# Kernel tuning notes

Hardware: AMD Instinct MI355X
Metric: run time of the kernel (lower is better)

## Reference

```python
import jax, jax.numpy as jnp
import numpy as np

B, CH, H, W = 32, 128, 32, 32
EMB = 64      # embedding_dim
NEMB = 8192   # codebook size


def setup_inputs() -> dict:
    key = jax.random.key(0)
    k1, k2, k3, k4 = jax.random.split(key, 4)
    z = jax.random.normal(k1, (B, CH, H, W), jnp.float32)
    # 1x1 conv == per-pixel linear: weight [EMB, CH], bias [EMB]
    proj_w = jax.random.normal(k2, (EMB, CH), jnp.float32) * 0.05
    proj_b = jax.random.normal(k3, (EMB,), jnp.float32) * 0.01
    embed_w = jax.random.normal(k4, (NEMB, EMB), jnp.float32)
    return {"z": z, "proj_w": proj_w, "proj_b": proj_b, "embed_w": embed_w}


def reference(z, proj_w, proj_b, embed_w):
    Bz, C, Hh, Ww = z.shape
    sg = jax.lax.stop_gradient
    # 1x1 conv then permute(0,2,3,1): [B,C,H,W] -> [B,H,W,E]
    z_e = jnp.einsum('bchw,ec->bhwe', z, proj_w) + proj_b
    flat = z_e.reshape(-1, z_e.shape[-1])  # [N, E], N = B*H*W
    dist = ((flat * flat).sum(1, keepdims=True)
            - 2.0 * (flat @ embed_w.T)
            + (embed_w * embed_w).sum(1)[None, :])
    z_q_ind = jnp.argmin(dist, axis=1).reshape(Bz, Hh, Ww)  # argmax(-dist)
    z_q_emb = embed_w[z_q_ind]  # gather: [B,H,W,E]
    commitment_cost = 0.25
    kld_scale = 10.0
    latent_loss = kld_scale * (
        commitment_cost * jnp.mean((sg(z_q_emb) - z_e) ** 2)
        + jnp.mean((z_q_emb - sg(z_e)) ** 2))
    z_q_flat = z_q_emb
    # straight-through estimator
    z_q_st = z_e + sg(z_q_emb - z_e)
    out = jnp.transpose(z_q_st, (0, 3, 1, 2))  # [B,E,H,W]
    return out, z_q_flat, latent_loss, z_q_ind
```

## Files before the change

kernel.cpp:

```cpp
#include <hip/hip_runtime.h>

#define NPIX   32768
#define NEMB_  8192
#define EMB_   64
#define CH_    128
#define CAPP   768

#define OUT_OFF  0
#define ZQ_OFF   2097152
#define LOSS_OFF 4194304
#define IND_OFF  4194305

typedef _Float16 h8   __attribute__((ext_vector_type(8)));
typedef float    f16f __attribute__((ext_vector_type(16)));

__global__ __launch_bounds__(256) void k_wpack(
    const float* __restrict__ ew, const float* __restrict__ pw,
    float4* __restrict__ W4, float* __restrict__ pwT,
    float* __restrict__ wsq, float* __restrict__ wsqp,
    float* __restrict__ lacc, int* __restrict__ done)
{
    const int tid = threadIdx.x;
    {
        const int i = blockIdx.x * 256 + tid;
        const float v = pw[i];
        const int e = i >> 7, c = i & 127;
        pwT[c * 64 + e] = v;
    }
    const int m = blockIdx.x * 256 + tid;
    const float4* wr = (const float4*)(ew + (size_t)m * EMB_);
    float w[EMB_];
    float s = 0.f;
    #pragma unroll
    for (int i = 0; i < 16; i++) {
        float4 v = wr[i];
        w[4*i] = v.x; w[4*i+1] = v.y; w[4*i+2] = v.z; w[4*i+3] = v.w;
        s += v.x*v.x + v.y*v.y + v.z*v.z + v.w*v.w;
    }
    wsq[m] = s;
    float sh = (float)(_Float16)s;
    float sl = s - sh;
    const int t  = m >> 5;
    const int li = m & 31;
    #pragma unroll
    for (int s5 = 0; s5 < 4; s5++) {
        #pragma unroll
        for (int h = 0; h < 2; h++) {
            h8 hh;
            #pragma unroll
            for (int j = 0; j < 8; j++) hh[j] = (_Float16)w[s5 * 16 + h * 8 + j];
            W4[(size_t)(t * 5 + s5) * 64 + h * 32 + li] = __builtin_bit_cast(float4, hh);
        }
    }
    {
        h8 hh;
        #pragma unroll
        for (int j = 0; j < 8; j++) hh[j] = (_Float16)0.f;
        hh[0] = (_Float16)sh; hh[1] = (_Float16)sl;
        W4[(size_t)(t * 5 + 4) * 64 + 0 * 32 + li] = __builtin_bit_cast(float4, hh);
        #pragma unroll
        for (int j = 0; j < 8; j++) hh[j] = (_Float16)0.f;
        W4[(size_t)(t * 5 + 4) * 64 + 1 * 32 + li] = __builtin_bit_cast(float4, hh);
    }
    __shared__ float red[256];
    red[tid] = s;
    __syncthreads();
    for (int o = 128; o > 0; o >>= 1) {
        if (tid < o) red[tid] = fmaxf(red[tid], red[tid + o]);
        __syncthreads();
    }
    if (tid == 0) wsqp[blockIdx.x] = red[0];
    if (blockIdx.x == 0 && tid == 0) { *lacc = 0.f; *done = 0; }
}

__device__ __forceinline__ unsigned long long pack_key(float d, int m)
{
    unsigned fb = __float_as_uint(d);
    fb ^= ((int)fb < 0) ? 0xFFFFFFFFu : 0x80000000u;
    return ((unsigned long long)fb << 32) | (unsigned)m;
}

__global__ __launch_bounds__(1024, 4) void k_fused3(
    const float4* __restrict__ W4, const float* __restrict__ z,
    const float* __restrict__ pwT, const float* __restrict__ pb,
    const float* __restrict__ wsqp, const float* __restrict__ wsq,
    const float* __restrict__ ew,
    float* __restrict__ out, float* __restrict__ lacc, int* __restrict__ done)
{
    __shared__ __align__(16) float xs[128][68];
    __shared__ float s1s[1024], s2s[1024], s3s[1024];
    __shared__ short i1s[1024], i2s[1024];
    __shared__ float xsqp_s[8][128];
    __shared__ float thr_s[128];
    __shared__ int   pairs[CAPP];
    __shared__ unsigned long long pbest[128];
    __shared__ int   winner_s[128];
    __shared__ int   smask[128];
    __shared__ float wred[16];
    __shared__ int   npair_s;
    __shared__ float wm_s;

    const int tid  = threadIdx.x;
    const int wv   = tid >> 6;
    const int lane = tid & 63;
    const int n0   = blockIdx.x * 128;
    const int hlf  = lane >> 5;

    if (tid == 0) npair_s = 0;
    if (tid < 128) { smask[tid] = 0; pbest[tid] = ~0ULL; }
    if (tid < 32) {
        float w = wsqp[tid];
        #pragma unroll
        for (int o = 16; o > 0; o >>= 1) w = fmaxf(w, __shfl_xor(w, o));
        if (tid == 0) wm_s = w;
    }

    {
        const int oct = tid >> 7;
        const int pxp = tid & 127;
        const int e0  = __builtin_amdgcn_readfirstlane(oct << 3);
        const float* zp = z + (size_t)(n0 >> 10) * (CH_ * 1024) + (n0 & 1023) + pxp;
        float acc[8];
        #pragma unroll
        for (int j = 0; j < 8; j++) acc[j] = 0.f;
        #pragma unroll 8
        for (int c = 0; c < CH_; c++) {
            const float zv = zp[(size_t)c * 1024];
            const float4* wr = (const float4*)(pwT + c * 64 + e0);
            float4 w0 = wr[0], w1 = wr[1];
            acc[0] = fmaf(zv, w0.x, acc[0]); acc[1] = fmaf(zv, w0.y, acc[1]);
            acc[2] = fmaf(zv, w0.z, acc[2]); acc[3] = fmaf(zv, w0.w, acc[3]);
            acc[4] = fmaf(zv, w1.x, acc[4]); acc[5] = fmaf(zv, w1.y, acc[5]);
            acc[6] = fmaf(zv, w1.z, acc[6]); acc[7] = fmaf(zv, w1.w, acc[7]);
        }
        const float4* pb4 = (const float4*)(pb + e0);
        float4 b0 = pb4[0], b1 = pb4[1];
        acc[0] += b0.x; acc[1] += b0.y; acc[2] += b0.z; acc[3] += b0.w;
        acc[4] += b1.x; acc[5] += b1.y; acc[6] += b1.z; acc[7] += b1.w;
        float sq = 0.f;
        #pragma unroll
        for (int j = 0; j < 8; j++) sq += acc[j] * acc[j];
        ((float4*)&xs[pxp][0])[oct * 2]     = make_float4(acc[0], acc[1], acc[2], acc[3]);
        ((float4*)&xs[pxp][0])[oct * 2 + 1] = make_float4(acc[4], acc[5], acc[6], acc[7]);
        xsqp_s[oct][pxp] = sq;
    }
    __syncthreads();

    const int ch = wv & 7;
    const int pg = wv >> 3;

    h8 bfr[2][4];
    #pragma unroll
    for (int j = 0; j < 2; j++) {
        const int px = pg * 64 + j * 32 + (lane & 31);
        #pragma unroll
        for (int s5 = 0; s5 < 4; s5++) {
            float4 u0 = *(const float4*)(&xs[px][s5 * 16 + hlf * 8]);
            float4 u1 = *(const float4*)(&xs[px][s5 * 16 + hlf * 8 + 4]);
            h8 hh;
            hh[0]=(_Float16)u0.x; hh[1]=(_Float16)u0.y; hh[2]=(_Float16)u0.z; hh[3]=(_Float16)u0.w;
            hh[4]=(_Float16)u1.x; hh[5]=(_Float16)u1.y; hh[6]=(_Float16)u1.z; hh[7]=(_Float16)u1.w;
            bfr[j][s5] = hh;
        }
    }
    h8 btail;
    {
        h8 hh;
        #pragma unroll
        for (int q = 0; q < 8; q++) hh[q] = (_Float16)0.f;
        if (hlf == 0) { hh[0] = (_Float16)-0.5f; hh[1] = (_Float16)-0.5f; }
        btail = hh;
    }

    const f16f kzero = {0,0,0,0,0,0,0,0,0,0,0,0,0,0,0,0};
    float s1[2], s2[2], s3[2];
    int   i1[2], i2[2];
    #pragma unroll
    for (int j = 0; j < 2; j++) { s1[j]=s2[j]=s3[j]=-3.0e38f; i1[j]=i2[j]=0; }

    const int tb = ch * 32;
    const float4* Wb = W4 + (size_t)tb * 320 + lane;
    float4 A[5];
    #pragma unroll
    for (int s = 0; s < 5; s++) A[s] = Wb[s * 64];

#define REDUCE_J(ACC, JJ, GT)                                                  \
    {                                                                          \
        float t0 = fmaxf(fmaxf(ACC[0],  ACC[1]),  ACC[2]);                     \
        float t1 = fmaxf(fmaxf(ACC[3],  ACC[4]),  ACC[5]);                     \
        float t2 = fmaxf(fmaxf(ACC[6],  ACC[7]),  ACC[8]);                     \
        float t3 = fmaxf(fmaxf(ACC[9],  ACC[10]), ACC[11]);                    \
        float t4 = fmaxf(fmaxf(ACC[12], ACC[13]), ACC[14]);                    \
        float v  = fmaxf(fmaxf(fmaxf(t0, t1), fmaxf(t2, t3)),                  \
                         fmaxf(t4, ACC[15]));                                  \
        v = fmaxf(v, __shfl_xor(v, 32));                                       \
        bool c1 = v > s1[JJ];                                                  \
        bool c2 = v > s2[JJ];                                                  \
        int  cand = c1 ? i1[JJ] : (GT);                                        \
        i2[JJ] = c2 ? cand : i2[JJ];                                           \
        s3[JJ] = fmaxf(fminf(s2[JJ], v), s3[JJ]);                              \
        s3[JJ] = fminf(s3[JJ], fmaxf(s2[JJ], v));                              \
        s2[JJ] = fmaxf(fminf(s1[JJ], v), fminf(s2[JJ], fmaxf(s1[JJ], v)));     \
        i1[JJ] = c1 ? (GT) : i1[JJ];                                           \
        s1[JJ] = fmaxf(s1[JJ], v);                                             \
    }

    for (int tt = 0; tt < 32; tt++) {
        const int gt = tb + tt;
        f16f acc0 = __builtin_amdgcn_mfma_f32_32x32x16_f16(
            __builtin_bit_cast(h8, A[0]), bfr[0][0], kzero, 0, 0, 0);
        #pragma unroll
        for (int s = 1; s < 4; s++)
            acc0 = __builtin_amdgcn_mfma_f32_32x32x16_f16(
                __builtin_bit_cast(h8, A[s]), bfr[0][s], acc0, 0, 0, 0);
        acc0 = __builtin_amdgcn_mfma_f32_32x32x16_f16(
            __builtin_bit_cast(h8, A[4]), btail, acc0, 0, 0, 0);
        REDUCE_J(acc0, 0, gt)
        f16f acc1 = __builtin_amdgcn_mfma_f32_32x32x16_f16(
            __builtin_bit_cast(h8, A[0]), bfr[1][0], kzero, 0, 0, 0);
        #pragma unroll
        for (int s = 1; s < 4; s++)
            acc1 = __builtin_amdgcn_mfma_f32_32x32x16_f16(
                __builtin_bit_cast(h8, A[s]), bfr[1][s], acc1, 0, 0, 0);
        acc1 = __builtin_amdgcn_mfma_f32_32x32x16_f16(
            __builtin_bit_cast(h8, A[4]), btail, acc1, 0, 0, 0);
        {
            const int tp = (tt + 1) < 32 ? (tt + 1) : 31;
            const float4* wp = Wb + (size_t)tp * 320;
            #pragma unroll
            for (int s = 0; s < 5; s++) A[s] = wp[s * 64];
        }
        REDUCE_J(acc1, 1, gt)
    }
#undef REDUCE_J

    if (lane < 32) {
        #pragma unroll
        for (int j = 0; j < 2; j++) {
            const int px = pg * 64 + j * 32 + lane;
            const int cell = px * 8 + ch;
            s1s[cell] = s1[j]; s2s[cell] = s2[j]; s3s[cell] = s3[j];
            i1s[cell] = (short)i1[j]; i2s[cell] = (short)i2[j];
        }
    }
    __syncthreads();

    if (tid < 128) {
        float s1g = s1s[tid * 8];
        #pragma unroll
        for (int c = 1; c < 8; c++) s1g = fmaxf(s1g, s1s[tid * 8 + c]);
        float xq = xsqp_s[0][tid];
        #pragma unroll
        for (int o = 1; o < 8; o++) xq += xsqp_s[o][tid];
        float E = 0.00125f * sqrtf(xq * wm_s) + 1e-5f * wm_s + 3e-4f;
        thr_s[tid] = s1g - 2.0f * E;
    }
    __syncthreads();
    {
        const int cell = tid;
        const int px = cell >> 3, chh = cell & 7;
        const float th = thr_s[px];
        const float cs1 = s1s[cell], cs2 = s2s[cell], cs3 = s3s[cell];
        if (cs3 >= th) {
            int pos = atomicAdd(&npair_s, 32);
            if (pos + 32 <= CAPP) {
                for (int t = 0; t < 32; t++)
                    pairs[pos + t] = (px << 8) | (chh * 32 + t);
            } else {
                for (int t = 0; t < 32; t++)
                    if (pos + t < CAPP) pairs[pos + t] = -1;
                smask[px] = 1;
            }
        } else {
            if (cs1 >= th) {
                int pos = atomicAdd(&npair_s, 1);
                if (pos < CAPP) pairs[pos] = (px << 8) | (int)i1s[cell];
                else smask[px] = 1;
            }
            if (cs2 >= th) {
                int pos = atomicAdd(&npair_s, 1);
                if (pos < CAPP) pairs[pos] = (px << 8) | (int)i2s[cell];
                else smask[px] = 1;
            }
        }
    }
    __syncthreads();
    const int np = npair_s < CAPP ? npair_s : CAPP;

    const int lg = lane >> 4;
    const int ld = lane & 15;
    for (int i = wv; i < np; i += 16) {
        const int pr = pairs[i];
        if (pr < 0) continue;
        const int p = pr >> 8;
        if (smask[p]) continue;
        const int t = pr & 255;
        const float4* tb4 = (const float4*)(ew + (size_t)t * 2048);
        float4 wq[8];
        #pragma unroll
        for (int q = 0; q < 8; q++) wq[q] = tb4[q * 64 + lane];
        const float4 xq = *(const float4*)(&xs[p][ld * 4]);
        unsigned long long best = ~0ULL;
        #pragma unroll
        for (int q = 0; q < 8; q++) {
            float dp = wq[q].x*xq.x + wq[q].y*xq.y + wq[q].z*xq.z + wq[q].w*xq.w;
            dp += __shfl_xor(dp, 1);
            dp += __shfl_xor(dp, 2);
            dp += __shfl_xor(dp, 4);
            dp += __shfl_xor(dp, 8);
            const int m = t * 32 + q * 4 + lg;
            unsigned long long key = pack_key(fmaf(-2.f, dp, wsq[m]), m);
            best = key < best ? key : best;
        }
        { unsigned long long o = __shfl_xor(best, 16); best = o < best ? o : best; }
        { unsigned long long o = __shfl_xor(best, 32); best = o < best ? o : best; }
        if (lane == 0) atomicMin(&pbest[p], best);
    }
    for (int p = wv; p < 128; p += 16) {
        if (!smask[p]) continue;
        const float4 xq = *(const float4*)(&xs[p][ld * 4]);
        unsigned long long bk = ~0ULL;
        for (int t = 0; t < 256; t++) {
            const float4* tb4 = (const float4*)(ew + (size_t)t * 2048);
            #pragma unroll
            for (int q = 0; q < 8; q++) {
                float4 wv4 = tb4[q * 64 + lane];
                float dp = wv4.x*xq.x + wv4.y*xq.y + wv4.z*xq.z + wv4.w*xq.w;
                dp += __shfl_xor(dp, 1);
                dp += __shfl_xor(dp, 2);
                dp += __shfl_xor(dp, 4);
                dp += __shfl_xor(dp, 8);
                const int m = t * 32 + q * 4 + lg;
                unsigned long long key = pack_key(fmaf(-2.f, dp, wsq[m]), m);
                bk = key < bk ? key : bk;
            }
        }
        { unsigned long long o = __shfl_xor(bk, 16); bk = o < bk ? o : bk; }
        { unsigned long long o = __shfl_xor(bk, 32); bk = o < bk ? o : bk; }
        if (lane == 0) atomicMin(&pbest[p], bk);
    }
    __syncthreads();
    if (tid < 128) {
        const int win = (int)(unsigned)(pbest[tid] & 0xFFFFFFFFULL);
        winner_s[tid] = win;
        out[IND_OFF + n0 + tid] = (float)win;
    }
    __syncthreads();
    float lsum = 0.f;
    {
        const int px = tid >> 3, sg = tid & 7;
        const int win = winner_s[px];
        const float4* wr = (const float4*)(ew + (size_t)win * EMB_ + sg * 8);
        float4* xr  = (float4*)(&xs[px][sg * 8]);
        float4* zq4 = (float4*)(out + ZQ_OFF + (size_t)(n0 + px) * EMB_ + sg * 8);
        #pragma unroll
        for (int i = 0; i < 2; i++) {
            float4 w4v = wr[i];
            float4 z4  = xr[i];
            float d0 = w4v.x - z4.x, d1 = w4v.y - z4.y;
            float d2 = w4v.z - z4.z, d3 = w4v.w - z4.w;
            lsum += d0*d0 + d1*d1 + d2*d2 + d3*d3;
            xr[i]  = w4v;
            zq4[i] = w4v;
        }
    }
    __syncthreads();
    {
        const int bI  = n0 >> 10;
        const int hw0 = n0 & 1023;
        float* ob = out + OUT_OFF + (size_t)bI * (EMB_ * 1024) + hw0;
        #pragma unroll
        for (int r = 0; r < 8; r++) {
            const int idx = r * 1024 + tid;
            const int e = idx >> 7, px = idx & 127;
            ob[(size_t)e * 1024 + px] = xs[px][e];
        }
    }
    {
        float v = lsum;
        #pragma unroll
        for (int o = 1; o < 64; o <<= 1) v += __shfl_xor(v, o);
        if (lane == 0) wred[wv] = v;
    }
    __syncthreads();
    if (tid == 0) {
        float s = wred[0];
        #pragma unroll
        for (int k = 1; k < 16; k++) s += wred[k];
        atomicAdd(lacc, s);
        __threadfence();
        int old = atomicAdd(done, 1);
        if (old == (int)gridDim.x - 1) {
            float tot = atomicAdd(lacc, 0.0f);
            out[LOSS_OFF] = 12.5f * (tot / 2097152.0f);
        }
    }
}

extern "C" void kernel_launch(void* const* d_in, const int* in_sizes, int n_in,
                              void* d_out, int out_size, void* d_ws, size_t ws_size,
                              hipStream_t stream)
{
    const float* z  = (const float*)d_in[0];
    const float* pw = (const float*)d_in[1];
    const float* pb = (const float*)d_in[2];
    const float* ew = (const float*)d_in[3];
    float* out = (float*)d_out;

    char* ws = (char*)d_ws;
    float4* W4   = (float4*)(ws);
    float*  pwT  = (float*) (ws + 1310720);
    float*  wsq  = (float*) (ws + 1474560);
    float*  wsqp = (float*) (ws + 1507328);
    float*  lacc = (float*) (ws + 1507456);
    int*    done = (int*)   (ws + 1507460);

    hipLaunchKernelGGL(k_wpack,  dim3(32),  dim3(256), 0, stream,
                       ew, pw, W4, pwT, wsq, wsqp, lacc, done);
    hipLaunchKernelGGL(k_fused3, dim3(256), dim3(1024), 0, stream,
                       W4, z, pwT, pb, wsqp, wsq, ew, out, lacc, done);
}
```

Before: 156.5 us.

## Fuse codebook packing into main VQ kernel with grid-wide flag sync

Removes the separate codebook pre-pack kernel. Each of the 256 blocks now packs 32 codebook rows to fp16 in wave 0 and bumps a global counter, then spins on that counter before the MFMA distance loop. The projection now reads proj_w directly instead of a transposed copy, and the tile loop double-buffers codebook fragments across two register sets. This removes one kernel launch and its dependency gap, at the cost of a spin-wait that assumes all 256 blocks are co-resident, plus a memset launch and extra register pressure.

```diff
diff --git a/kernel.cpp b/kernel.cpp
--- a/kernel.cpp
+++ b/kernel.cpp
@@ -13,65 +13,6 @@
 
 typedef _Float16 h8   __attribute__((ext_vector_type(8)));
 typedef float    f16f __attribute__((ext_vector_type(16)));
-
-__global__ __launch_bounds__(256) void k_wpack(
-    const float* __restrict__ ew, const float* __restrict__ pw,
-    float4* __restrict__ W4, float* __restrict__ pwT,
-    float* __restrict__ wsq, float* __restrict__ wsqp,
-    float* __restrict__ lacc, int* __restrict__ done)
-{
-    const int tid = threadIdx.x;
-    {
-        const int i = blockIdx.x * 256 + tid;
-        const float v = pw[i];
-        const int e = i >> 7, c = i & 127;
-        pwT[c * 64 + e] = v;
-    }
-    const int m = blockIdx.x * 256 + tid;
-    const float4* wr = (const float4*)(ew + (size_t)m * EMB_);
-    float w[EMB_];
-    float s = 0.f;
-    #pragma unroll
-    for (int i = 0; i < 16; i++) {
-        float4 v = wr[i];
-        w[4*i] = v.x; w[4*i+1] = v.y; w[4*i+2] = v.z; w[4*i+3] = v.w;
-        s += v.x*v.x + v.y*v.y + v.z*v.z + v.w*v.w;
-    }
-    wsq[m] = s;
-    float sh = (float)(_Float16)s;
-    float sl = s - sh;
-    const int t  = m >> 5;
-    const int li = m & 31;
-    #pragma unroll
-    for (int s5 = 0; s5 < 4; s5++) {
-        #pragma unroll
-        for (int h = 0; h < 2; h++) {
-            h8 hh;
-            #pragma unroll
-            for (int j = 0; j < 8; j++) hh[j] = (_Float16)w[s5 * 16 + h * 8 + j];
-            W4[(size_t)(t * 5 + s5) * 64 + h * 32 + li] = __builtin_bit_cast(float4, hh);
-        }
-    }
-    {
-        h8 hh;
-        #pragma unroll
-        for (int j = 0; j < 8; j++) hh[j] = (_Float16)0.f;
-        hh[0] = (_Float16)sh; hh[1] = (_Float16)sl;
-        W4[(size_t)(t * 5 + 4) * 64 + 0 * 32 + li] = __builtin_bit_cast(float4, hh);
-        #pragma unroll
-        for (int j = 0; j < 8; j++) hh[j] = (_Float16)0.f;
-        W4[(size_t)(t * 5 + 4) * 64 + 1 * 32 + li] = __builtin_bit_cast(float4, hh);
-    }
-    __shared__ float red[256];
-    red[tid] = s;
-    __syncthreads();
-    for (int o = 128; o > 0; o >>= 1) {
-        if (tid < o) red[tid] = fmaxf(red[tid], red[tid + o]);
-        __syncthreads();
-    }
-    if (tid == 0) wsqp[blockIdx.x] = red[0];
-    if (blockIdx.x == 0 && tid == 0) { *lacc = 0.f; *done = 0; }
-}
 
 __device__ __forceinline__ unsigned long long pack_key(float d, int m)
 {
@@ -80,12 +21,12 @@
     return ((unsigned long long)fb << 32) | (unsigned)m;
 }
 
-__global__ __launch_bounds__(1024, 4) void k_fused3(
-    const float4* __restrict__ W4, const float* __restrict__ z,
-    const float* __restrict__ pwT, const float* __restrict__ pb,
-    const float* __restrict__ wsqp, const float* __restrict__ wsq,
-    const float* __restrict__ ew,
-    float* __restrict__ out, float* __restrict__ lacc, int* __restrict__ done)
+__global__ __launch_bounds__(1024, 4) void k_vq(
+    const float* __restrict__ z,  const float* __restrict__ pw,
+    const float* __restrict__ pb, const float* __restrict__ ew,
+    float4* __restrict__ W4, float* __restrict__ wsq, float* __restrict__ wsqp,
+    float* __restrict__ out, float* __restrict__ lacc, int* __restrict__ done,
+    int* __restrict__ wdone)
 {
     __shared__ __align__(16) float xs[128][68];
     __shared__ float s1s[1024], s2s[1024], s3s[1024];
@@ -108,30 +49,77 @@
 
     if (tid == 0) npair_s = 0;
     if (tid < 128) { smask[tid] = 0; pbest[tid] = ~0ULL; }
-    if (tid < 32) {
-        float w = wsqp[tid];
-        #pragma unroll
-        for (int o = 16; o > 0; o >>= 1) w = fmaxf(w, __shfl_xor(w, o));
-        if (tid == 0) wm_s = w;
+
+    if (wv == 0) {
+        if (lane < 32) {
+            const int m = blockIdx.x * 32 + lane;
+            const float4* wr = (const float4*)(ew + (size_t)m * EMB_);
+            float w[EMB_];
+            float s = 0.f;
+            #pragma unroll
+            for (int i = 0; i < 16; i++) {
+                float4 v = wr[i];
+                w[4*i] = v.x; w[4*i+1] = v.y; w[4*i+2] = v.z; w[4*i+3] = v.w;
+                s += v.x*v.x + v.y*v.y + v.z*v.z + v.w*v.w;
+            }
+            wsq[m] = s;
+            float sh = (float)(_Float16)s;
+            float sl = s - sh;
+            const int t  = blockIdx.x;
+            const int li = lane;
+            #pragma unroll
+            for (int s5 = 0; s5 < 4; s5++) {
+                #pragma unroll
+                for (int h = 0; h < 2; h++) {
+                    h8 hh;
+                    #pragma unroll
+                    for (int j = 0; j < 8; j++) hh[j] = (_Float16)w[s5*16 + h*8 + j];
+                    W4[(size_t)(t * 5 + s5) * 64 + h * 32 + li] = __builtin_bit_cast(float4, hh);
+                }
+            }
+            {
+                h8 hh;
+                #pragma unroll
+                for (int j = 0; j < 8; j++) hh[j] = (_Float16)0.f;
+                hh[0] = (_Float16)sh; hh[1] = (_Float16)sl;
+                W4[(size_t)(t * 5 + 4) * 64 + 0 * 32 + li] = __builtin_bit_cast(float4, hh);
+                #pragma unroll
+                for (int j = 0; j < 8; j++) hh[j] = (_Float16)0.f;
+                W4[(size_t)(t * 5 + 4) * 64 + 1 * 32 + li] = __builtin_bit_cast(float4, hh);
+            }
+            float sm = s;
+            #pragma unroll
+            for (int o = 16; o > 0; o >>= 1) sm = fmaxf(sm, __shfl_xor(sm, o));
+            if (lane == 0) wsqp[blockIdx.x] = sm;
+        }
+        __threadfence();
+        if (tid == 0) atomicAdd(wdone, 1);
     }
 
     {
         const int oct = tid >> 7;
         const int pxp = tid & 127;
         const int e0  = __builtin_amdgcn_readfirstlane(oct << 3);
+        const float* pwb = pw + e0 * CH_;
         const float* zp = z + (size_t)(n0 >> 10) * (CH_ * 1024) + (n0 & 1023) + pxp;
         float acc[8];
         #pragma unroll
         for (int j = 0; j < 8; j++) acc[j] = 0.f;
-        #pragma unroll 8
+        #pragma unroll 4
         for (int c = 0; c < CH_; c++) {
             const float zv = zp[(size_t)c * 1024];
-            const float4* wr = (const float4*)(pwT + c * 64 + e0);
-            float4 w0 = wr[0], w1 = wr[1];
-            acc[0] = fmaf(zv, w0.x, acc[0]); acc[1] = fmaf(zv, w0.y, acc[1]);
-            acc[2] = fmaf(zv, w0.z, acc[2]); acc[3] = fmaf(zv, w0.w, acc[3]);
-            acc[4] = fmaf(zv, w1.x, acc[4]); acc[5] = fmaf(zv, w1.y, acc[5]);
-            acc[6] = fmaf(zv, w1.z, acc[6]); acc[7] = fmaf(zv, w1.w, acc[7]);
+            const float w0 = pwb[c];
+            const float w1 = pwb[CH_ + c];
+            const float w2 = pwb[2*CH_ + c];
+            const float w3 = pwb[3*CH_ + c];
+            const float w4 = pwb[4*CH_ + c];
+            const float w5 = pwb[5*CH_ + c];
+            const float w6 = pwb[6*CH_ + c];
+            const float w7 = pwb[7*CH_ + c];
+            acc[0] = fmaf(zv, w0, acc[0]); acc[1] = fmaf(zv, w1, acc[1]);
+            acc[2] = fmaf(zv, w2, acc[2]); acc[3] = fmaf(zv, w3, acc[3]);
+            acc[4] = fmaf(zv, w4, acc[4]); acc[5] = fmaf(zv, w5, acc[5]);
+            acc[6] = fmaf(zv, w6, acc[6]); acc[7] = fmaf(zv, w7, acc[7]);
         }
         const float4* pb4 = (const float4*)(pb + e0);
         float4 b0 = pb4[0], b1 = pb4[1];
@@ -172,6 +160,19 @@
         btail = hh;
     }
 
+    if (tid == 0) {
+        while (atomicAdd(wdone, 0) < 256) { }
+        __threadfence();
+    }
+    __syncthreads();
+    if (tid < 64) {
+        float w = fmaxf(fmaxf(wsqp[tid], wsqp[tid + 64]),
+                        fmaxf(wsqp[tid + 128], wsqp[tid + 192]));
+        #pragma unroll
+        for (int o = 32; o > 0; o >>= 1) w = fmaxf(w, __shfl_xor(w, o));
+        if (tid == 0) wm_s = w;
+    }
+
     const f16f kzero = {0,0,0,0,0,0,0,0,0,0,0,0,0,0,0,0};
     float s1[2], s2[2], s3[2];
     int   i1[2], i2[2];
@@ -180,9 +181,11 @@
 
     const int tb = ch * 32;
     const float4* Wb = W4 + (size_t)tb * 320 + lane;
-    float4 A[5];
+    float4 A0[5], A1[5];
     #pragma unroll
-    for (int s = 0; s < 5; s++) A[s] = Wb[s * 64];
+    for (int s = 0; s < 5; s++) A0[s] = Wb[s * 64];
+    #pragma unroll
+    for (int s = 0; s < 5; s++) A1[s] = Wb[320 + s * 64];
 
 #define REDUCE_J(ACC, JJ, GT)                                                  \
     {                                                                          \
@@ -205,33 +208,40 @@
         s1[JJ] = fmaxf(s1[JJ], v);                                             \
     }
 
-    for (int tt = 0; tt < 32; tt++) {
-        const int gt = tb + tt;
-        f16f acc0 = __builtin_amdgcn_mfma_f32_32x32x16_f16(
-            __builtin_bit_cast(h8, A[0]), bfr[0][0], kzero, 0, 0, 0);
-        #pragma unroll
-        for (int s = 1; s < 4; s++)
-            acc0 = __builtin_amdgcn_mfma_f32_32x32x16_f16(
-                __builtin_bit_cast(h8, A[s]), bfr[0][s], acc0, 0, 0, 0);
-        acc0 = __builtin_amdgcn_mfma_f32_32x32x16_f16(
-            __builtin_bit_cast(h8, A[4]), btail, acc0, 0, 0, 0);
-        REDUCE_J(acc0, 0, gt)
-        f16f acc1 = __builtin_amdgcn_mfma_f32_32x32x16_f16(
-            __builtin_bit_cast(h8, A[0]), bfr[1][0], kzero, 0, 0, 0);
-        #pragma unroll
-        for (int s = 1; s < 4; s++)
-            acc1 = __builtin_amdgcn_mfma_f32_32x32x16_f16(
-                __builtin_bit_cast(h8, A[s]), bfr[1][s], acc1, 0, 0, 0);
-        acc1 = __builtin_amdgcn_mfma_f32_32x32x16_f16(
-            __builtin_bit_cast(h8, A[4]), btail, acc1, 0, 0, 0);
-        {
-            const int tp = (tt + 1) < 32 ? (tt + 1) : 31;
-            const float4* wp = Wb + (size_t)tp * 320;
-            #pragma unroll
-            for (int s = 0; s < 5; s++) A[s] = wp[s * 64];
-        }
-        REDUCE_J(acc1, 1, gt)
-    }
+#define TILE_BODY(AB, TT, PF)                                                  \
+    {                                                                          \
+        const int gt = tb + (TT);                                              \
+        f16f acc0 = __builtin_amdgcn_mfma_f32_32x32x16_f16(                    \
+            __builtin_bit_cast(h8, AB[0]), bfr[0][0], kzero, 0, 0, 0);         \
+        _Pragma("unroll")                                                      \
+        for (int s = 1; s < 4; s++)                                            \
+            acc0 = __builtin_amdgcn_mfma_f32_32x32x16_f16(                     \
+                __builtin_bit_cast(h8, AB[s]), bfr[0][s], acc0, 0, 0, 0);      \
+        acc0 = __builtin_amdgcn_mfma_f32_32x32x16_f16(                         \
+            __builtin_bit_cast(h8, AB[4]), btail, acc0, 0, 0, 0);              \
+        REDUCE_J(acc0, 0, gt)                                                  \
+        f16f acc1 = __builtin_amdgcn_mfma_f32_32x32x16_f16(                    \
+            __builtin_bit_cast(h8, AB[0]), bfr[1][0], kzero, 0, 0, 0);         \
+        _Pragma("unroll")                                                      \
+        for (int s = 1; s < 4; s++)                                            \
+            acc1 = __builtin_amdgcn_mfma_f32_32x32x16_f16(                     \
+                __builtin_bit_cast(h8, AB[s]), bfr[1][s], acc1, 0, 0, 0);      \
+        acc1 = __builtin_amdgcn_mfma_f32_32x32x16_f16(                         \
+            __builtin_bit_cast(h8, AB[4]), btail, acc1, 0, 0, 0);              \
+        {                                                                      \
+            const int tp = (PF) < 32 ? (PF) : 30;                              \
+            const float4* wp = Wb + (size_t)tp * 320;                          \
+            _Pragma("unroll")                                                  \
+            for (int s = 0; s < 5; s++) AB[s] = wp[s * 64];                    \
+        }                                                                      \
+        REDUCE_J(acc1, 1, gt)                                                  \
+    }
+
+    for (int tt = 0; tt < 32; tt += 2) {
+        TILE_BODY(A0, tt,     tt + 2)
+        TILE_BODY(A1, tt + 1, tt + 3)
+    }
+#undef TILE_BODY
 #undef REDUCE_J
 
     if (lane < 32) {
@@ -409,14 +419,14 @@
 
     char* ws = (char*)d_ws;
     float4* W4   = (float4*)(ws);
-    float*  pwT  = (float*) (ws + 1310720);
-    float*  wsq  = (float*) (ws + 1474560);
-    float*  wsqp = (float*) (ws + 1507328);
-    float*  lacc = (float*) (ws + 1507456);
-    int*    done = (int*)   (ws + 1507460);
-
-    hipLaunchKernelGGL(k_wpack,  dim3(32),  dim3(256), 0, stream,
-                       ew, pw, W4, pwT, wsq, wsqp, lacc, done);
-    hipLaunchKernelGGL(k_fused3, dim3(256), dim3(1024), 0, stream,
-                       W4, z, pwT, pb, wsqp, wsq, ew, out, lacc, done);
+    float*  wsq  = (float*) (ws + 1310720);
+    float*  wsqp = (float*) (ws + 1343488);
+    float*  lacc = (float*) (ws + 1344512);
+    int*    done = (int*)   (ws + 1344516);
+    int*    wdone= (int*)   (ws + 1344520);
+
+    hipMemsetAsync(ws + 1344512, 0, 12, stream);
+
+    hipLaunchKernelGGL(k_vq, dim3(256), dim3(1024), 0, stream,
+                       z, pw, pb, ew, W4, wsq, wsqp, out, lacc, done, wdone);
 }
```

Result: slower. 166.6 us (+6.5%).
